# Optimization experiments

Hardware: AMD Instinct MI355X
Metric: run time of the kernel (lower is better)

## Reference

```python
import jax, jax.numpy as jnp
import numpy as np

NB_RADIUSES = 24
SIGMA = 0.1


def setup_inputs() -> dict:
    key = jax.random.key(0)
    k1, k2, k3 = jax.random.split(key, 3)
    nb, nf, nx, ny, nz = 2, 2, 256, 256, 16
    x = jax.random.uniform(k1, (nb, nf, nx, ny, nz), dtype=jnp.float32)
    # center of mass: real part is the column coordinate (in [0, ny)),
    # imag part is the row coordinate (in [0, nx)) -- keep centers inside the plane
    com_real = jax.random.uniform(k2, (nb, nf, nz), dtype=jnp.float32) * ny
    com_imag = jax.random.uniform(k3, (nb, nf, nz), dtype=jnp.float32) * nx
    return {"x": x, "com_real": com_real, "com_imag": com_imag}


def reference(x, com_real, com_imag):
    nb, nf, nx, ny, nz = x.shape
    # complex plan: real = index % ny (column), imag = index // ny (row)
    col = jnp.arange(ny, dtype=jnp.float32)   # real axis
    row = jnp.arange(nx, dtype=jnp.float32)   # imag axis
    # centered plan, broadcast to (nb, nf, nx, ny, nz)
    dx = col[None, None, None, :, None] - com_real[:, :, None, None, :]
    dy = row[None, None, :, None, None] - com_imag[:, :, None, None, :]
    theta = jnp.arctan2(dy, dx)           # arg(centered_plan)
    theta_neg = jnp.arctan2(-dy, -dx)     # arg(-centered_plan)

    # angles i*(2pi/nr) - pi; branch selection identical to the torch code
    angles = np.arange(NB_RADIUSES) * (2.0 * np.pi / NB_RADIUSES) - np.pi
    use_neg = (angles > 0.5 * np.pi) | (angles < -0.5 * np.pi)
    targets = np.where(angles > 0.5 * np.pi, angles - np.pi,
                       np.where(angles < -0.5 * np.pi, angles + np.pi, angles))
    use_neg = jnp.asarray(use_neg)
    targets = jnp.asarray(targets.astype(np.float32))

    # select angle field per radius: (R, nb, nf, nx, ny, nz)
    sel = jnp.where(use_neg[:, None, None, None, None, None],
                    theta_neg[None], theta[None])
    coef = jnp.float32(1.0 / (SIGMA * np.sqrt(2.0 * np.pi)))
    diff = sel - targets[:, None, None, None, None, None]
    w = coef * jnp.exp(-(diff ** 2) / jnp.float32(2.0 * SIGMA ** 2))

    # gaussian-weighted reduction over the (x, y) plane, keep z
    s = jnp.einsum('Rbfxyz,bfxyz->bfRz', w, x)
    return jnp.sqrt(2.0 * s)
```

## Files before the change

### kernel.cpp

```cpp
#include <hip/hip_runtime.h>

#define NR 24
#define NBATCH 2
#define NFEAT 2
#define NX 256
#define NY 256
#define NZ 16
#define PAD 25
#define NBLK_PER_BF 512
#define NPART (NR * NZ)

__global__ __launch_bounds__(256) void grx_partial(
    const float* __restrict__ x,
    const float* __restrict__ com_real,
    const float* __restrict__ com_imag,
    float* __restrict__ ws)
{
    __shared__ float red[256 * PAD];

    const int tid  = threadIdx.x;
    const int z    = tid & 15;
    const int c0   = tid >> 4;
    const int half = blockIdx.x & 1;
    const int row  = (blockIdx.x >> 1) & (NX - 1);
    const int bf   = blockIdx.x >> 9;

    float* myred = &red[tid * PAD];
    #pragma unroll
    for (int i = 0; i < PAD; ++i) myred[i] = 0.0f;

    const float comr = com_real[bf * NZ + z];
    const float comi = com_imag[bf * NZ + z];
    const float dyv  = (float)row - comi;
    const float ady  = fabsf(dyv);

    const float PIF   = 3.14159265358979f;
    const float PI_2  = 1.57079632679490f;
    const float C_PSI = 3.81971863420549f;
    const float C_E   = -3.4269908169872414f;

    const float* xp = x + ((size_t)(bf * NX + row)) * (NY * NZ);

    #pragma unroll 2
    for (int kk = 0; kk < 8; ++kk) {
        const int col  = c0 + ((half * 8 + kk) << 4);
        const float xv = xp[col * NZ + z];
        const float dxv = (float)col - comr;

        const float adx = fabsf(dxv);
        const float mn  = fminf(adx, ady);
        const float mx  = fmaxf(adx, ady);
        const float t   = mn * __builtin_amdgcn_rcpf(fmaxf(mx, 1e-30f));
        const float r2  = t * t;
        float p = fmaf(r2, 0.0208351f, -0.0851330f);
        p = fmaf(r2, p, 0.1801410f);
        p = fmaf(r2, p, -0.3302995f);
        p = fmaf(r2, p, 0.9998660f);
        float th = t * p;
        if (ady > adx)  th = PI_2 - th;
        if (dxv < 0.0f) th = PIF - th;
        th = copysignf(th, dyv);

        const float psi = th * C_PSI;
        const float nf  = rintf(psi);
        const float f   = psi - nf;
        const int base  = (int)nf + 12;

        const float fm = f + 1.0f;
        const float fp = f - 1.0f;
        const float w0 = __expf(C_E * f  * f ) * xv;
        const float wm = __expf(C_E * fm * fm) * xv;
        const float wp = __expf(C_E * fp * fp) * xv;

        int v0 = base - 1; v0 = (v0 < 0)   ? v0 + 24 : v0;
        int v1 = base;     v1 = (v1 >= 24) ? v1 - 24 : v1;
        int v2 = base + 1; v2 = (v2 >= 24) ? v2 - 24 : v2;

        myred[v0] += wm;
        myred[v1] += w0;
        myred[v2] += wp;
    }

    __syncthreads();

    float* wsb = ws + (size_t)blockIdx.x * NPART;
    for (int o = tid; o < NPART; o += 256) {
        const int r  = o >> 4;
        const int zz = o & 15;
        float s = 0.0f;
        #pragma unroll
        for (int c = 0; c < 16; ++c)
            s += red[(c * 16 + zz) * PAD + r];
        wsb[o] = s;
    }
}

__global__ __launch_bounds__(256) void grx_reduce(
    const float* __restrict__ ws, float* __restrict__ out)
{
    const int b  = blockIdx.x;
    const int bf = b / NPART;
    const int o  = b - bf * NPART;
    const int tid = threadIdx.x;

    const float* base = ws + (size_t)bf * NBLK_PER_BF * NPART + o;
    float s = base[(size_t)tid * NPART] + base[(size_t)(tid + 256) * NPART];

    #pragma unroll
    for (int off = 32; off; off >>= 1) s += __shfl_down(s, off, 64);

    __shared__ float w4[4];
    if ((tid & 63) == 0) w4[tid >> 6] = s;
    __syncthreads();
    if (tid == 0) {
        const float coef = 3.9894228040143270f;
        const float tot = w4[0] + w4[1] + w4[2] + w4[3];
        out[b] = sqrtf(2.0f * coef * tot);
    }
}

extern "C" void kernel_launch(void* const* d_in, const int* in_sizes, int n_in,
                              void* d_out, int out_size, void* d_ws, size_t ws_size,
                              hipStream_t stream)
{
    const float* x  = (const float*)d_in[0];
    const float* cr = (const float*)d_in[1];
    const float* ci = (const float*)d_in[2];
    float* out = (float*)d_out;
    float* ws  = (float*)d_ws;

    grx_partial<<<dim3(NBATCH * NFEAT * NBLK_PER_BF), dim3(256), 0, stream>>>(x, cr, ci, ws);
    grx_reduce<<<dim3(NBATCH * NFEAT * NPART), dim3(256), 0, stream>>>(ws, out);
}
```

Baseline: 78.83 us.

## Fold angle scaling into atan poly, drop modular bins, transpose workspace

Rescales the atan polynomial coefficients so they output the radius-bin coordinate directly, removing a multiply and the constant pi offsets. The modular wraparound of bin indices is replaced by padding each thread's shared histogram to 27 slots, with the wrapped slots folded back during the block reduction. The loop is fully unrolled with a strength-reduced pointer and column offset. The workspace is transposed so the second-pass reduction reads contiguous memory instead of strided loads, at the cost of strided writes from the first kernel.

Result: faster. 77.11 us (-2.2%).

```diff
diff --git a/kernel.cpp b/kernel.cpp
--- a/kernel.cpp
+++ b/kernel.cpp
@@ -6,7 +6,7 @@
 #define NX 256
 #define NY 256
 #define NZ 16
-#define PAD 25
+#define PAD 27
 #define NBLK_PER_BF 512
 #define NPART (NR * NZ)
 
@@ -34,77 +34,78 @@
     const float dyv  = (float)row - comi;
     const float ady  = fabsf(dyv);
 
-    const float PIF   = 3.14159265358979f;
-    const float PI_2  = 1.57079632679490f;
-    const float C_PSI = 3.81971863420549f;
-    const float C_E   = -3.4269908169872414f;
+    const float A4 = 0.0795845f;
+    const float A3 = -0.3251843f;
+    const float A2 = 0.6880875f;
+    const float A1 = -1.2616510f;
+    const float A0 = 3.8192070f;
+    const float C_E = -3.4269908169872414f;
 
-    const float* xp = x + ((size_t)(bf * NX + row)) * (NY * NZ);
+    const float* xq = x + ((size_t)(bf * NX + row)) * (NY * NZ)
+                        + ((c0 + (half << 7)) * NZ + z);
+    float dxv = (float)(c0 + (half << 7)) - comr;
 
-    #pragma unroll 2
+    #pragma unroll
     for (int kk = 0; kk < 8; ++kk) {
-        const int col  = c0 + ((half * 8 + kk) << 4);
-        const float xv = xp[col * NZ + z];
-        const float dxv = (float)col - comr;
+        const float xv = xq[kk * 256];
 
         const float adx = fabsf(dxv);
         const float mn  = fminf(adx, ady);
         const float mx  = fmaxf(adx, ady);
         const float t   = mn * __builtin_amdgcn_rcpf(fmaxf(mx, 1e-30f));
         const float r2  = t * t;
-        float p = fmaf(r2, 0.0208351f, -0.0851330f);
-        p = fmaf(r2, p, 0.1801410f);
-        p = fmaf(r2, p, -0.3302995f);
-        p = fmaf(r2, p, 0.9998660f);
-        float th = t * p;
-        if (ady > adx)  th = PI_2 - th;
-        if (dxv < 0.0f) th = PIF - th;
-        th = copysignf(th, dyv);
+        float p = fmaf(r2, A4, A3);
+        p = fmaf(r2, p, A2);
+        p = fmaf(r2, p, A1);
+        p = fmaf(r2, p, A0);
+        float psi = t * p;
+        if (ady > adx)  psi = 6.0f - psi;
+        if (dxv < 0.0f) psi = 12.0f - psi;
+        psi = copysignf(psi, dyv);
+        dxv += 16.0f;
 
-        const float psi = th * C_PSI;
         const float nf  = rintf(psi);
         const float f   = psi - nf;
         const int base  = (int)nf + 12;
 
         const float fm = f + 1.0f;
         const float fp = f - 1.0f;
+        const float wm = __expf(C_E * fm * fm) * xv;
         const float w0 = __expf(C_E * f  * f ) * xv;
-        const float wm = __expf(C_E * fm * fm) * xv;
         const float wp = __expf(C_E * fp * fp) * xv;
 
-        int v0 = base - 1; v0 = (v0 < 0)   ? v0 + 24 : v0;
-        int v1 = base;     v1 = (v1 >= 24) ? v1 - 24 : v1;
-        int v2 = base + 1; v2 = (v2 >= 24) ? v2 - 24 : v2;
-
-        myred[v0] += wm;
-        myred[v1] += w0;
-        myred[v2] += wp;
+        myred[base]     += wm;
+        myred[base + 1] += w0;
+        myred[base + 2] += wp;
     }
 
     __syncthreads();
 
-    float* wsb = ws + (size_t)blockIdx.x * NPART;
+    const int l = blockIdx.x & (NBLK_PER_BF - 1);
     for (int o = tid; o < NPART; o += 256) {
         const int r  = o >> 4;
         const int zz = o & 15;
         float s = 0.0f;
         #pragma unroll
-        for (int c = 0; c < 16; ++c)
-            s += red[(c * 16 + zz) * PAD + r];
-        wsb[o] = s;
+        for (int c = 0; c < 16; ++c) {
+            const float* rr = &red[(c * 16 + zz) * PAD];
+            float v = rr[r + 1];
+            if (r == 0)  v += rr[25];
+            if (r == 1)  v += rr[26];
+            if (r == 23) v += rr[0];
+            s += v;
+        }
+        ws[((size_t)(bf * NPART + o) * NBLK_PER_BF) + l] = s;
     }
 }
 
 __global__ __launch_bounds__(256) void grx_reduce(
     const float* __restrict__ ws, float* __restrict__ out)
 {
-    const int b  = blockIdx.x;
-    const int bf = b / NPART;
-    const int o  = b - bf * NPART;
+    const int b   = blockIdx.x;
     const int tid = threadIdx.x;
-
-    const float* base = ws + (size_t)bf * NBLK_PER_BF * NPART + o;
-    float s = base[(size_t)tid * NPART] + base[(size_t)(tid + 256) * NPART];
+    const float* base = ws + (size_t)b * NBLK_PER_BF;
+    float s = base[tid] + base[tid + 256];
 
     #pragma unroll
     for (int off = 32; off; off >>= 1) s += __shfl_down(s, off, 64);
@@ -113,9 +114,7 @@
     if ((tid & 63) == 0) w4[tid >> 6] = s;
     __syncthreads();
     if (tid == 0) {
-        const float coef = 3.9894228040143270f;
-        const float tot = w4[0] + w4[1] + w4[2] + w4[3];
-        out[b] = sqrtf(2.0f * coef * tot);
+        out[b] = sqrtf(7.9788456080286535f * (w4[0] + w4[1] + w4[2] + w4[3]));
     }
 }
 
```
